# Kernel tuning notes

Measured on AMD Instinct MI355X. Metric: run time of the kernel, lower is better.

## Reference

```python
import jax, jax.numpy as jnp
import numpy as np

B, S, M, H, P, T = 32, 400, 400, 200, 16, 4

def setup_inputs() -> dict:
    key = jax.random.key(0)
    ks = jax.random.split(key, 20)
    sc = 0.05
    inp = {
        'att': jax.random.normal(ks[0], (B, S, M), jnp.float32),
        'mod': jax.random.normal(ks[1], (B, S, M), jnp.float32),
        'mask': jnp.ones((B, S), jnp.float32),
        # LSTMCell: input 2*M, hidden H, gate order i,f,g,o
        'lstm_Wih': jax.random.normal(ks[2], (4 * H, 2 * M), jnp.float32) * sc,
        'lstm_Whh': jax.random.normal(ks[3], (4 * H, H), jnp.float32) * sc,
        'lstm_bih': jnp.zeros((4 * H,), jnp.float32),
        'lstm_bhh': jnp.zeros((4 * H,), jnp.float32),
    }
    for pfx, off in (('s', 4), ('e', 11)):
        inp[pfx + '_rW'] = jax.random.normal(ks[off + 0], (H, 2 * M + H), jnp.float32) * sc
        inp[pfx + '_W1'] = jax.random.normal(ks[off + 1], (P * H, M + H), jnp.float32) * sc
        inp[pfx + '_b1'] = jnp.zeros((P * H,), jnp.float32)
        inp[pfx + '_W2'] = jax.random.normal(ks[off + 2], (P * H, H), jnp.float32) * sc
        inp[pfx + '_b2'] = jnp.zeros((P * H,), jnp.float32)
        inp[pfx + '_W3'] = jax.random.normal(ks[off + 3], (P, 2 * H), jnp.float32) * sc
        inp[pfx + '_b3'] = jnp.zeros((P,), jnp.float32)
    return inp

def _gather(mod, idx):
    # mod:[B,S,M], idx:[B] -> [B,M]
    return jnp.take_along_axis(mod, idx[:, None, None], axis=1)[:, 0, :]

def _lstm_cell(x, h, c, Wih, Whh, bih, bhh):
    g = x @ Wih.T + bih + h @ Whh.T + bhh  # [B,4H]
    i, f, gg, o = jnp.split(g, 4, axis=1)
    c2 = jax.nn.sigmoid(f) * c + jax.nn.sigmoid(i) * jnp.tanh(gg)
    h2 = jax.nn.sigmoid(o) * jnp.tanh(c2)
    return h2, c2

def _hmn(mod, h, us, ue, mask, rW, W1, b1, W2, b2, W3, b3):
    r = jnp.tanh(jnp.concatenate([h, us, ue], 1) @ rW.T)  # [B,H]
    x = jnp.concatenate([mod, jnp.broadcast_to(r[:, None, :], (B, S, H))], 2)  # [B,S,M+H]
    m1 = (x @ W1.T + b1).reshape(B, S, P, H).max(2)   # maxout 1
    m2 = (m1 @ W2.T + b2).reshape(B, S, P, H).max(2)  # maxout 2
    logits = (jnp.concatenate([m1, m2], 2) @ W3.T + b3).max(2)  # [B,S]
    logits = jnp.where(mask > 0, logits, -1e30)
    return jax.nn.log_softmax(logits, axis=1)

def reference(att, mod, mask, lstm_Wih, lstm_Whh, lstm_bih, lstm_bhh,
              s_rW, s_W1, s_b1, s_W2, s_b2, s_W3, s_b3,
              e_rW, e_W1, e_b1, e_W2, e_b2, e_W3, e_b3):
    s_prev = jnp.zeros((B,), jnp.int32)
    e_prev = jnp.sum(mask, 1).astype(jnp.int32) - 1
    h = jnp.zeros((B, H), mod.dtype)
    c = jnp.zeros((B, H), mod.dtype)
    log_p1s, log_p2s = [], []
    for _ in range(T):
        u_s = _gather(mod, s_prev)
        u_e = _gather(mod, e_prev)
        h, c = _lstm_cell(jnp.concatenate([u_s, u_e], 1), h, c,
                          lstm_Wih, lstm_Whh, lstm_bih, lstm_bhh)
        lp1 = _hmn(mod, h, u_s, u_e, mask, s_rW, s_W1, s_b1, s_W2, s_b2, s_W3, s_b3)
        s_prev = jnp.argmax(lp1, axis=1).astype(jnp.int32)
        u_s = _gather(mod, s_prev)
        lp2 = _hmn(mod, h, u_s, u_e, mask, e_rW, e_W1, e_b1, e_W2, e_b2, e_W3, e_b3)
        e_prev = jnp.argmax(lp2, axis=1).astype(jnp.int32)
        log_p1s.append(lp1)
        log_p2s.append(lp2)
    return jnp.stack(log_p1s, 1), jnp.stack(log_p2s, 1)  # each [B,T,S]
```

## Files before the change

### kernel.cpp

```cpp
#include <hip/hip_runtime.h>
#include <math.h>

#define NB 32
#define NS 400
#define NM 400
#define NH 200
#define NP 16
#define NT 4
#define NBS (NB*NS)
#define NPH (NP*NH)
#define NPH2 3328
#define NJT 13
#define NX  (2*NM)
#define NG  (4*NH)
#define NR  (2*NM+NH)
#define K1  1280
#define K2  640

typedef __attribute__((ext_vector_type(8))) short short8v;
typedef __attribute__((ext_vector_type(4))) float f32x4;
typedef __attribute__((ext_vector_type(4))) unsigned short us4;
typedef unsigned short ushort;

__device__ __forceinline__ float sigf(float x){ return 1.0f/(1.0f+expf(-x)); }

__device__ __forceinline__ ushort f2bf(float x){
  union{float f; unsigned u;} v; v.f=x;
  unsigned r = v.u + 0x7fffu + ((v.u>>16)&1u);
  return (ushort)(r>>16);
}
__device__ __forceinline__ float bf2f(ushort u){
  union{float f; unsigned v;} x; x.v = ((unsigned)u)<<16; return x.f;
}
__device__ __forceinline__ float wave_sum(float v){
  #pragma unroll
  for (int o=32;o>0;o>>=1) v += __shfl_xor(v, o);
  return v;
}

__global__ __launch_bounds__(256) void init_kernel(const float* __restrict__ mask,
    float* __restrict__ h, float* __restrict__ c,
    int* __restrict__ sprev, int* __restrict__ eprev){
  int b = blockIdx.x, tid = threadIdx.x;
  __shared__ float red[256];
  float s = 0.f;
  for (int i=tid;i<NS;i+=256) s += mask[(size_t)b*NS+i];
  red[tid]=s; __syncthreads();
  for (int st=128;st>0;st>>=1){ if(tid<st) red[tid]+=red[tid+st]; __syncthreads(); }
  if (tid==0){ sprev[b]=0; eprev[b]=(int)red[0]-1; }
  for (int i=tid;i<NH;i+=256){ h[(size_t)b*NH+i]=0.f; c[(size_t)b*NH+i]=0.f; }
}

__global__ __launch_bounds__(256) void conv_mod_k(const float* __restrict__ in, ushort* __restrict__ out){
  for (size_t i = (size_t)blockIdx.x*256+threadIdx.x; i < (size_t)NBS*K1; i += (size_t)gridDim.x*256){
    int r = (int)(i/K1), k = (int)(i%K1);
    ushort v = 0;
    if (k < 3*NM){
      float x = in[(size_t)r*NM + (k % NM)];
      ushort h = f2bf(x);
      v = (k < NM || k >= 2*NM) ? h : f2bf(x - bf2f(h));
    }
    out[i] = v;
  }
}
__global__ __launch_bounds__(256) void conv_w1_k(const float* __restrict__ in, ushort* __restrict__ out){
  for (size_t i = (size_t)blockIdx.x*256+threadIdx.x; i < (size_t)NPH2*K1; i += (size_t)gridDim.x*256){
    int jp = (int)(i/K1), k = (int)(i%K1);
    ushort v = 0;
    if (jp < NPH && k < 3*NM){
      int j = (jp&15)*NH + (jp>>4);
      float x = in[(size_t)j*(NM+NH) + (k % NM)];
      ushort h = f2bf(x);
      v = (k < 2*NM) ? h : f2bf(x - bf2f(h));
    }
    out[i] = v;
  }
}
__global__ __launch_bounds__(256) void conv_w2_k(const float* __restrict__ in, ushort* __restrict__ out){
  for (size_t i = (size_t)blockIdx.x*256+threadIdx.x; i < (size_t)NPH2*K2; i += (size_t)gridDim.x*256){
    int jp = (int)(i/K2), k = (int)(i%K2);
    ushort v = 0;
    if (jp < NPH && k < 3*NH){
      int j = (jp&15)*NH + (jp>>4);
      float x = in[(size_t)j*NH + (k % NH)];
      ushort h = f2bf(x);
      v = (k < 2*NH) ? h : f2bf(x - bf2f(h));
    }
    out[i] = v;
  }
}
__global__ __launch_bounds__(256) void conv_w1r_k(const float* __restrict__ in, float* __restrict__ out){
  for (size_t i = (size_t)blockIdx.x*256+threadIdx.x; i < (size_t)NH*NPH; i += (size_t)gridDim.x*256){
    int k = (int)(i/NPH), jp = (int)(i%NPH);
    int hh = jp>>4, p = jp&15, j = p*NH + hh;
    out[i] = in[(size_t)j*(NM+NH) + NM + k];
  }
}
__global__ __launch_bounds__(256) void permv_k(const float* __restrict__ in, float* __restrict__ out){
  int i = blockIdx.x*256+threadIdx.x;
  if (i < NPH) out[(i%NH)*NP + i/NH] = in[i];
  else if (i < NPH2) out[i] = 0.f;
}
__global__ __launch_bounds__(256) void pad_zero_k(ushort* __restrict__ p, int stride, int start, int width, int rows){
  for (size_t i = (size_t)blockIdx.x*256+threadIdx.x; i < (size_t)rows*width; i += (size_t)gridDim.x*256){
    int r = (int)(i/width), j = (int)(i%width);
    p[(size_t)r*stride + start + j] = 0;
  }
}

__global__ __launch_bounds__(256) void lstm_gates(const float* __restrict__ mod,
    const int* __restrict__ sprev, const int* __restrict__ eprev,
    const float* __restrict__ h,
    const float* __restrict__ Wih, const float* __restrict__ Whh,
    const float* __restrict__ bih, const float* __restrict__ bhh,
    float* __restrict__ gs){
  int b=blockIdx.x, tid=threadIdx.x;
  __shared__ float xs[NX+NH];
  const float* us = mod + ((size_t)b*NS + sprev[b])*NM;
  const float* ue = mod + ((size_t)b*NS + eprev[b])*NM;
  for (int i=tid;i<NM;i+=256){ xs[i]=us[i]; xs[NM+i]=ue[i]; }
  for (int i=tid;i<NH;i+=256) xs[NX+i]=h[(size_t)b*NH+i];
  __syncthreads();
  int w=tid>>6, lane=tid&63;
  int j = blockIdx.y*4 + w;
  const float* wih = Wih + (size_t)j*NX;
  const float* whh = Whh + (size_t)j*NH;
  float acc=0.f;
  for (int k=lane;k<NX;k+=64) acc += xs[k]*wih[k];
  for (int k=lane;k<NH;k+=64) acc += xs[NX+k]*whh[k];
  acc = wave_sum(acc);
  if (lane==0) gs[(size_t)b*NG+j] = acc + bih[j] + bhh[j];
}
__global__ __launch_bounds__(256) void lstm_update(const float* __restrict__ gs,
    float* __restrict__ h, float* __restrict__ c){
  int b=blockIdx.x, j=threadIdx.x;
  if (j<NH){
    float iv=gs[(size_t)b*NG+j], fv=gs[(size_t)b*NG+NH+j];
    float gv=gs[(size_t)b*NG+2*NH+j], ov=gs[(size_t)b*NG+3*NH+j];
    float c2 = sigf(fv)*c[(size_t)b*NH+j] + sigf(iv)*tanhf(gv);
    c[(size_t)b*NH+j]=c2;
    h[(size_t)b*NH+j]=sigf(ov)*tanhf(c2);
  }
}

__global__ __launch_bounds__(256) void r_kernel(const float* __restrict__ mod,
    const int* __restrict__ sprev, const int* __restrict__ eprev,
    const float* __restrict__ h, const float* __restrict__ rW,
    float* __restrict__ rbuf){
  int b=blockIdx.x, tid=threadIdx.x;
  __shared__ float zs[NR];
  const float* us = mod + ((size_t)b*NS + sprev[b])*NM;
  const float* ue = mod + ((size_t)b*NS + eprev[b])*NM;
  for (int i=tid;i<NH;i+=256) zs[i]=h[(size_t)b*NH+i];
  for (int i=tid;i<NM;i+=256){ zs[NH+i]=us[i]; zs[NH+NM+i]=ue[i]; }
  __syncthreads();
  int w=tid>>6, lane=tid&63;
  int j = blockIdx.y*4 + w;
  const float* wr = rW + (size_t)j*NR;
  float acc=0.f;
  for (int k=lane;k<NR;k+=64) acc += zs[k]*wr[k];
  acc = wave_sum(acc);
  if (lane==0) rbuf[(size_t)b*NH+j] = tanhf(acc);
}

__global__ __launch_bounds__(256) void prer_kernel(const float* __restrict__ rbuf,
    const float* __restrict__ W1rT, const float* __restrict__ b1p,
    float* __restrict__ prer){
  int b=blockIdx.x, tid=threadIdx.x;
  __shared__ float rs[NH];
  if (tid < NH) rs[tid] = rbuf[(size_t)b*NH+tid];
  __syncthreads();
  int jp = blockIdx.y*256 + tid;
  if (jp < NPH2){
    float acc = 0.f;
    if (jp < NPH){
      acc = b1p[jp];
      #pragma unroll 8
      for (int k=0;k<NH;k++) acc += rs[k]*W1rT[(size_t)k*NPH + jp];
    }
    prer[(size_t)b*NPH2 + jp] = acc;
  }
}

template<int MODE>
__global__ __launch_bounds__(512, 2) void gemm_fused(
    const ushort* __restrict__ A, const ushort* __restrict__ W,
    const float* __restrict__ bias, void* __restrict__ outp, int itb){
  constexpr int LDK = (MODE==1) ? K2 : K1;
  constexpr int NTI = LDK/32;
  __shared__ __align__(16) ushort As[4][256*32];
  __shared__ __align__(16) ushort Bs[4][256*32];
  __shared__ float biasLds[2][256];
  __shared__ float outT[256][16];
  const int tid = threadIdx.x;
  const int nwg = gridDim.x;
  const int q = nwg >> 3, r = nwg & 7;
  const int xcd = blockIdx.x & 7, sub = blockIdx.x >> 3;
  const int wkid = (xcd < r) ? (xcd*(q+1) + sub) : (r*(q+1) + (xcd-r)*q + sub);
  const int i0 = (itb + wkid / NJT) * 256, j0 = (wkid % NJT) * 256;
  const int b0 = i0/NS;
  if (MODE==0){
    if (tid<256) biasLds[0][tid] = bias[(size_t)b0*NPH2 + j0 + tid];
    else { int b1r=(i0+255)/NS; biasLds[1][tid-256] = bias[(size_t)b1r*NPH2 + j0 + (tid-256)]; }
  } else if (MODE==1){
    if (tid<256) biasLds[0][tid] = bias[j0+tid];
  }
  const int w = tid>>6, l = tid&63;
  const int wr = w>>2, wc = w&3;
  const int fr = l&15, fk = l>>4;
  const int srow = w*32 + (l>>2);
  const int sslot = l&3;
  const int swzc = (sslot ^ ((srow>>1)&3))*8;
  const ushort* gA0 = A + (size_t)(i0+srow)*LDK + swzc;
  const ushort* gB0 = W + (size_t)(j0+srow)*LDK + swzc;
  const int ldsOff = srow*32 + sslot*8;
  auto stage = [&](int slot, int kt){
    const ushort* a = gA0 + kt*32;
    const ushort* b = gB0 + kt*32;
    __builtin_amdgcn_global_load_lds((const __attribute__((address_space(1))) void*)a,
        (__attribute__((address_space(3))) void*)(&As[slot][ldsOff]), 16, 0, 0);
    __builtin_amdgcn_global_load_lds((const __attribute__((address_space(1))) void*)(a + 16*LDK),
        (__attribute__((address_space(3))) void*)(&As[slot][ldsOff + 16*32]), 16, 0, 0);
    __builtin_amdgcn_global_load_lds((const __attribute__((address_space(1))) void*)b,
        (__attribute__((address_space(3))) void*)(&Bs[slot][ldsOff]), 16, 0, 0);
    __builtin_amdgcn_global_load_lds((const __attribute__((address_space(1))) void*)(b + 16*LDK),
        (__attribute__((address_space(3))) void*)(&Bs[slot][ldsOff + 16*32]), 16, 0, 0);
  };
  f32x4 acc[8][4] = {};
  stage(0,0); stage(1,1); stage(2,2);
  for (int t=0; t<NTI; t++){
    if (t+2 < NTI)      asm volatile("s_waitcnt vmcnt(8)\n\ts_barrier" ::: "memory");
    else if (t+1 < NTI) asm volatile("s_waitcnt vmcnt(4)\n\ts_barrier" ::: "memory");
    else                asm volatile("s_waitcnt vmcnt(0)\n\ts_barrier" ::: "memory");
    const int s = t&3;
    short8v a[8], b[4];
    #pragma unroll
    for (int m=0;m<8;m++){
      int row = wr*128 + m*16 + fr;
      a[m] = *(const short8v*)&As[s][row*32 + ((fk ^ ((row>>1)&3))*8)];
    }
    #pragma unroll
    for (int n=0;n<4;n++){
      int row = wc*64 + n*16 + fr;
      b[n] = *(const short8v*)&Bs[s][row*32 + ((fk ^ ((row>>1)&3))*8)];
    }
    if (t+3 < NTI) stage((t+3)&3, t+3);
    __builtin_amdgcn_s_setprio(1);
    #pragma unroll
    for (int m=0;m<8;m++)
      #pragma unroll
      for (int n=0;n<4;n++)
        acc[m][n] = __builtin_amdgcn_mfma_f32_16x16x32_bf16(a[m], b[n], acc[m][n], 0,0,0);
    __builtin_amdgcn_s_setprio(0);
  }
  if (MODE==2){
    float* o = (float*)outp;
    #pragma unroll
    for (int m=0;m<8;m++){
      #pragma unroll
      for (int n=0;n<4;n++){
        int col = j0 + wc*64 + n*16 + fr;
        if (col < NPH){
          int rbase = i0 + wr*128 + m*16 + fk*4;
          #pragma unroll
          for (int reg=0;reg<4;reg++)
            o[(size_t)(rbase+reg)*NPH + col] = acc[m][n][reg];
        }
      }
    }
    return;
  }
  __syncthreads();
  const int blim = (b0+1)*NS;
  #pragma unroll
  for (int m=0;m<8;m++){
    #pragma unroll
    for (int n=0;n<4;n++){
      int colL = wc*64 + n*16 + fr;
      int rbase = wr*128 + m*16 + fk*4;
      #pragma unroll
      for (int reg=0; reg<4; reg++){
        int rowL = rbase + reg;
        float bv = (MODE==0 && (i0+rowL) >= blim) ? biasLds[1][colL] : biasLds[0][colL];
        float v = acc[m][n][reg] + bv;
        v = fmaxf(v, __shfl_xor(v,1));
        v = fmaxf(v, __shfl_xor(v,2));
        v = fmaxf(v, __shfl_xor(v,4));
        v = fmaxf(v, __shfl_xor(v,8));
        if (fr==0) outT[rowL][wc*4+n] = v;
      }
    }
  }
  __syncthreads();
  {
    int rowL = tid>>1;
    int hloc0 = (tid&1)*8;
    int hg0 = (j0>>4) + hloc0;
    if (hg0 < NH){
      int absrow = i0 + rowL;
      float v[8];
      #pragma unroll
      for (int qq=0;qq<8;qq++) v[qq] = outT[rowL][hloc0+qq];
      if (MODE==0){
        ushort* o = (ushort*)outp + (size_t)absrow*K2 + hg0;
        ushort hi[8], lo[8];
        #pragma unroll
        for (int qq=0;qq<8;qq++){ hi[qq]=f2bf(v[qq]); lo[qq]=f2bf(v[qq]-bf2f(hi[qq])); }
        *(us4*)(o)        = (us4){hi[0],hi[1],hi[2],hi[3]};
        *(us4*)(o+4)      = (us4){hi[4],hi[5],hi[6],hi[7]};
        *(us4*)(o+NH)     = (us4){lo[0],lo[1],lo[2],lo[3]};
        *(us4*)(o+NH+4)   = (us4){lo[4],lo[5],lo[6],lo[7]};
        *(us4*)(o+2*NH)   = (us4){hi[0],hi[1],hi[2],hi[3]};
        *(us4*)(o+2*NH+4) = (us4){hi[4],hi[5],hi[6],hi[7]};
      } else {
        float* o = (float*)outp + (size_t)absrow*NH + hg0;
        *(f32x4*)o     = (f32x4){v[0],v[1],v[2],v[3]};
        *(f32x4*)(o+4) = (f32x4){v[4],v[5],v[6],v[7]};
      }
    }
  }
}

__global__ __launch_bounds__(256) void maxp_kernel(const float* __restrict__ premod,
    const float* __restrict__ prer, ushort* __restrict__ m1e){
  int i = blockIdx.x;
  int b = i / NS;
  int h = threadIdx.x;
  if (h >= NH) return;
  const float* pm = premod + (size_t)i*NPH + h*16;
  const float* pr = prer + (size_t)b*NPH2 + h*16;
  float v = -INFINITY;
  #pragma unroll
  for (int p=0;p<16;p+=4){
    f32x4 a = *(const f32x4*)(pm+p);
    f32x4 c = *(const f32x4*)(pr+p);
    v = fmaxf(v, fmaxf(fmaxf(a.x+c.x, a.y+c.y), fmaxf(a.z+c.z, a.w+c.w)));
  }
  ushort hi = f2bf(v), lo = f2bf(v - bf2f(hi));
  ushort* o = m1e + (size_t)i*K2;
  o[h] = hi; o[NH+h] = lo; o[2*NH+h] = hi;
}

__global__ __launch_bounds__(256) void logits_main(const ushort* __restrict__ m1e,
    const float* __restrict__ m2, const float* __restrict__ W3, const float* __restrict__ b3,
    const float* __restrict__ mask, float* __restrict__ lg){
  int b=blockIdx.x;
  int s=blockIdx.y*256+threadIdx.x;
  if (s >= NS) return;
  const ushort* a = m1e + (size_t)(b*NS+s)*K2;
  const float4* d = (const float4*)(m2 + (size_t)(b*NS+s)*NH);
  float acc[NP];
  #pragma unroll
  for (int p=0;p<NP;p++) acc[p]=b3[p];
  for (int k=0;k<NH/4;k++){
    us4 hv = *(const us4*)(a + 4*k);
    us4 lv = *(const us4*)(a + NH + 4*k);
    float4 dv = d[k];
    float a0=bf2f(hv.x)+bf2f(lv.x), a1=bf2f(hv.y)+bf2f(lv.y);
    float a2=bf2f(hv.z)+bf2f(lv.z), a3=bf2f(hv.w)+bf2f(lv.w);
    #pragma unroll
    for (int p=0;p<NP;p++){
      const float* wp = W3 + p*(2*NH) + 4*k;
      acc[p] += a0*wp[0]+a1*wp[1]+a2*wp[2]+a3*wp[3];
      const float* w2 = wp + NH;
      acc[p] += dv.x*w2[0]+dv.y*w2[1]+dv.z*w2[2]+dv.w*w2[3];
    }
  }
  float best=acc[0];
  #pragma unroll
  for (int p=1;p<NP;p++) best=fmaxf(best,acc[p]);
  lg[(size_t)b*NS+s] = (mask[(size_t)b*NS+s] > 0.f) ? best : -1e30f;
}

__global__ __launch_bounds__(256) void logits_fin(const float* __restrict__ lg,
    float* __restrict__ out, int t, int* __restrict__ prevIdx){
  int b=blockIdx.x, tid=threadIdx.x;
  __shared__ float rv[256]; __shared__ int ri[256]; __shared__ float sv[256];
  float bv=-INFINITY; int bi=NS;
  for (int s=tid;s<NS;s+=256){ float v=lg[(size_t)b*NS+s]; if (v>bv){bv=v;bi=s;} }
  rv[tid]=bv; ri[tid]=bi; __syncthreads();
  for (int st=128;st>0;st>>=1){
    if (tid<st){
      float v2=rv[tid+st]; int i2=ri[tid+st];
      if (v2>rv[tid] || (v2==rv[tid] && i2<ri[tid])){ rv[tid]=v2; ri[tid]=i2; }
    }
    __syncthreads();
  }
  float mx = rv[0];
  float ps=0.f;
  for (int s=tid;s<NS;s+=256) ps += expf(lg[(size_t)b*NS+s]-mx);
  sv[tid]=ps; __syncthreads();
  for (int st=128;st>0;st>>=1){ if (tid<st) sv[tid]+=sv[tid+st]; __syncthreads(); }
  float lse = mx + logf(sv[0]);
  for (int s=tid;s<NS;s+=256) out[((size_t)b*NT + t)*NS + s] = lg[(size_t)b*NS+s]-lse;
  if (tid==0) prevIdx[b]=ri[0];
}

extern "C" void kernel_launch(void* const* d_in, const int* in_sizes, int n_in,
                              void* d_out, int out_size, void* d_ws, size_t ws_size,
                              hipStream_t stream){
  const float* mod  = (const float*)d_in[1];
  const float* mask = (const float*)d_in[2];
  const float* Wih  = (const float*)d_in[3];
  const float* Whh  = (const float*)d_in[4];
  const float* bih  = (const float*)d_in[5];
  const float* bhh  = (const float*)d_in[6];
  const float* rW[2] = {(const float*)d_in[7],  (const float*)d_in[14]};
  const float* W1[2] = {(const float*)d_in[8],  (const float*)d_in[15]};
  const float* b1[2] = {(const float*)d_in[9],  (const float*)d_in[16]};
  const float* W2[2] = {(const float*)d_in[10], (const float*)d_in[17]};
  const float* b2[2] = {(const float*)d_in[11], (const float*)d_in[18]};
  const float* W3[2] = {(const float*)d_in[12], (const float*)d_in[19]};
  const float* b3[2] = {(const float*)d_in[13], (const float*)d_in[20]};
  float* out[2];
  out[0] = (float*)d_out;
  out[1] = out[0] + (size_t)NB*NT*NS;

  float* wsf = (float*)d_ws;
  size_t off = 0;
  auto carve = [&](size_t n)->size_t{ size_t o=off; off += (n + 63) & ~(size_t)63; return o; };
  float* hbuf   = wsf + carve((size_t)NB*NH);
  float* cbuf   = wsf + carve((size_t)NB*NH);
  float* prer   = wsf + carve((size_t)NB*NPH2);
  int*   sprev  = (int*)(wsf + carve(128));
  int*   eprev  = sprev + 32;
  float* m2f    = wsf + carve((size_t)NBS*NH);
  float* b2p[2] = {wsf + carve(NPH2), wsf + carve(NPH2)};
  float* b1p[2] = {wsf + carve(NPH2), wsf + carve(NPH2)};
  float* rbuf   = wsf + carve((size_t)NB*NH);
  float* gsbuf  = wsf + carve((size_t)NB*NG);
  float* lgbuf  = wsf + carve((size_t)NB*NS);
  float* W1rT[2]= {wsf + carve((size_t)NH*NPH), wsf + carve((size_t)NH*NPH)};
  ushort* modExp   = (ushort*)(wsf + carve((size_t)NBS*K1/2));
  ushort* W1exp[2] = {(ushort*)(wsf + carve((size_t)NPH2*K1/2)),
                      (ushort*)(wsf + carve((size_t)NPH2*K1/2))};
  ushort* W2exp[2] = {(ushort*)(wsf + carve((size_t)NPH2*K2/2)),
                      (ushort*)(wsf + carve((size_t)NPH2*K2/2))};
  ushort* m1exp    = (ushort*)(wsf + carve((size_t)NBS*K2/2));

  size_t availF = ws_size / 4;
  const size_t margin = 4096;
  int Xh[2] = {0, 0};
  float* premod[2] = {nullptr, nullptr};
  for (int net=0; net<2; net++){
    long rem = (long)availF - (long)off - (long)margin;
    long rows = rem > 0 ? rem / NPH : 0;
    rows = (rows / 256) * 256;
    if (rows > NBS) rows = NBS;
    if (rows >= 256){
      Xh[net] = (int)rows;
      premod[net] = wsf + carve((size_t)rows * NPH);
    }
  }

  init_kernel<<<NB, 256, 0, stream>>>(mask, hbuf, cbuf, sprev, eprev);
  conv_mod_k<<<2048, 256, 0, stream>>>(mod, modExp);
  pad_zero_k<<<256, 256, 0, stream>>>(m1exp, K2, 3*NH, K2-3*NH, NBS);
  for (int net=0; net<2; net++){
    conv_w1_k<<<2048, 256, 0, stream>>>(W1[net], W1exp[net]);
    conv_w2_k<<<1024, 256, 0, stream>>>(W2[net], W2exp[net]);
    conv_w1r_k<<<1024, 256, 0, stream>>>(W1[net], W1rT[net]);
    permv_k<<<(NPH2+255)/256, 256, 0, stream>>>(b2[net], b2p[net]);
    permv_k<<<(NPH2+255)/256, 256, 0, stream>>>(b1[net], b1p[net]);
  }
  for (int net=0; net<2; net++)
    if (Xh[net] > 0)
      gemm_fused<2><<<(Xh[net]/256)*NJT, 512, 0, stream>>>(modExp, W1exp[net], nullptr,
                                                           (void*)premod[net], 0);

  const int GFULL = (NBS/256) * NJT;
  for (int t=0; t<NT; t++){
    lstm_gates<<<dim3(NB, NG/4), 256, 0, stream>>>(mod, sprev, eprev, hbuf,
                                                   Wih, Whh, bih, bhh, gsbuf);
    lstm_update<<<NB, 256, 0, stream>>>(gsbuf, hbuf, cbuf);
    for (int net=0; net<2; net++){
      r_kernel<<<dim3(NB, NH/4), 256, 0, stream>>>(mod, sprev, eprev, hbuf, rW[net], rbuf);
      prer_kernel<<<dim3(NB, NPH2/256), 256, 0, stream>>>(rbuf, W1rT[net], b1p[net], prer);
      int X = Xh[net];
      if (X > 0)
        maxp_kernel<<<X, 256, 0, stream>>>(premod[net], prer, m1exp);
      if (X < NBS)
        gemm_fused<0><<<((NBS-X)/256)*NJT, 512, 0, stream>>>(modExp, W1exp[net], prer,
                                                             (void*)m1exp, X/256);
      gemm_fused<1><<<GFULL, 512, 0, stream>>>(m1exp, W2exp[net], b2p[net], (void*)m2f, 0);
      logits_main<<<dim3(NB, 2), 256, 0, stream>>>(m1exp, m2f, W3[net], b3[net], mask, lgbuf);
      logits_fin<<<NB, 256, 0, stream>>>(lgbuf, out[net], t, net==0 ? sprev : eprev);
    }
  }
}
```

Measured before the change: 2.771 ms.

## Store bf16 hi/lo split once and reuse A/W fragments across three MFMA products

The split-bf16 operands were stored as three concatenated segments (hi,lo,hi against hi,hi,lo), so the GEMM ran over K=3x. Now each operand keeps only hi and lo segments, and the GEMM loads both into LDS and issues the three cross products (a0*w0, a1*w0, a0*w1) from shared fragments. This cuts global and LDS traffic per unit of work and shrinks the workspace buffers. The pipeline depth drops from 4 to 2 stages and an extra barrier is added per iteration, and the outT buffer now shares its storage with the tiles.

```diff
diff --git a/kernel.cpp b/kernel.cpp
--- a/kernel.cpp
+++ b/kernel.cpp
@@ -14,8 +14,10 @@
 #define NX  (2*NM)
 #define NG  (4*NH)
 #define NR  (2*NM+NH)
-#define K1  1280
-#define K2  640
+#define SG1 416
+#define SK1 832
+#define SG2 224
+#define SK2 448
 
 typedef __attribute__((ext_vector_type(8))) short short8v;
 typedef __attribute__((ext_vector_type(4))) float f32x4;
@@ -52,39 +54,46 @@
 }
 
 __global__ __launch_bounds__(256) void conv_mod_k(const float* __restrict__ in, ushort* __restrict__ out){
-  for (size_t i = (size_t)blockIdx.x*256+threadIdx.x; i < (size_t)NBS*K1; i += (size_t)gridDim.x*256){
-    int r = (int)(i/K1), k = (int)(i%K1);
+  for (size_t i = (size_t)blockIdx.x*256+threadIdx.x; i < (size_t)NBS*SK1; i += (size_t)gridDim.x*256){
+    int r = (int)(i/SK1), k = (int)(i%SK1);
     ushort v = 0;
-    if (k < 3*NM){
-      float x = in[(size_t)r*NM + (k % NM)];
-      ushort h = f2bf(x);
-      v = (k < NM || k >= 2*NM) ? h : f2bf(x - bf2f(h));
+    if (k < 400){
+      float x = in[(size_t)r*NM + k]; v = f2bf(x);
+    } else if (k >= SG1 && k < SG1+400){
+      float x = in[(size_t)r*NM + (k-SG1)];
+      ushort h = f2bf(x); v = f2bf(x - bf2f(h));
     }
     out[i] = v;
   }
 }
 __global__ __launch_bounds__(256) void conv_w1_k(const float* __restrict__ in, ushort* __restrict__ out){
-  for (size_t i = (size_t)blockIdx.x*256+threadIdx.x; i < (size_t)NPH2*K1; i += (size_t)gridDim.x*256){
-    int jp = (int)(i/K1), k = (int)(i%K1);
+  for (size_t i = (size_t)blockIdx.x*256+threadIdx.x; i < (size_t)NPH2*SK1; i += (size_t)gridDim.x*256){
+    int jp = (int)(i/SK1), k = (int)(i%SK1);
     ushort v = 0;
-    if (jp < NPH && k < 3*NM){
+    if (jp < NPH){
       int j = (jp&15)*NH + (jp>>4);
-      float x = in[(size_t)j*(NM+NH) + (k % NM)];
-      ushort h = f2bf(x);
-      v = (k < 2*NM) ? h : f2bf(x - bf2f(h));
+      if (k < 400){
+        v = f2bf(in[(size_t)j*(NM+NH) + k]);
+      } else if (k >= SG1 && k < SG1+400){
+        float x = in[(size_t)j*(NM+NH) + (k-SG1)];
+        ushort h = f2bf(x); v = f2bf(x - bf2f(h));
+      }
     }
     out[i] = v;
   }
 }
 __global__ __launch_bounds__(256) void conv_w2_k(const float* __restrict__ in, ushort* __restrict__ out){
-  for (size_t i = (size_t)blockIdx.x*256+threadIdx.x; i < (size_t)NPH2*K2; i += (size_t)gridDim.x*256){
-    int jp = (int)(i/K2), k = (int)(i%K2);
+  for (size_t i = (size_t)blockIdx.x*256+threadIdx.x; i < (size_t)NPH2*SK2; i += (size_t)gridDim.x*256){
+    int jp = (int)(i/SK2), k = (int)(i%SK2);
     ushort v = 0;
-    if (jp < NPH && k < 3*NH){
+    if (jp < NPH){
       int j = (jp&15)*NH + (jp>>4);
-      float x = in[(size_t)j*NH + (k % NH)];
-      ushort h = f2bf(x);
-      v = (k < 2*NH) ? h : f2bf(x - bf2f(h));
+      if (k < 200){
+        v = f2bf(in[(size_t)j*NH + k]);
+      } else if (k >= SG2 && k < SG2+200){
+        float x = in[(size_t)j*NH + (k-SG2)];
+        ushort h = f2bf(x); v = f2bf(x - bf2f(h));
+      }
     }
     out[i] = v;
   }
@@ -186,12 +195,14 @@
 __global__ __launch_bounds__(512, 2) void gemm_fused(
     const ushort* __restrict__ A, const ushort* __restrict__ W,
     const float* __restrict__ bias, void* __restrict__ outp, int itb){
-  constexpr int LDK = (MODE==1) ? K2 : K1;
-  constexpr int NTI = LDK/32;
-  __shared__ __align__(16) ushort As[4][256*32];
-  __shared__ __align__(16) ushort Bs[4][256*32];
+  constexpr int SEG = (MODE==1) ? SG2 : SG1;
+  constexpr int LDK = 2*SEG;
+  constexpr int NKT = SEG/32;
+  struct SMs { ushort A0[2][256*32]; ushort A1[2][256*32];
+               ushort W0[2][256*32]; ushort W1[2][256*32]; };
+  union SMu { SMs s; float outT[256][16]; };
+  __shared__ SMu sm;
   __shared__ float biasLds[2][256];
-  __shared__ float outT[256][16];
   const int tid = threadIdx.x;
   const int nwg = gridDim.x;
   const int q = nwg >> 3, r = nwg & 7;
@@ -211,47 +222,78 @@
   const int srow = w*32 + (l>>2);
   const int sslot = l&3;
   const int swzc = (sslot ^ ((srow>>1)&3))*8;
-  const ushort* gA0 = A + (size_t)(i0+srow)*LDK + swzc;
-  const ushort* gB0 = W + (size_t)(j0+srow)*LDK + swzc;
+  const ushort* gA = A + (size_t)(i0+srow)*LDK + swzc;
+  const ushort* gB = W + (size_t)(j0+srow)*LDK + swzc;
   const int ldsOff = srow*32 + sslot*8;
   auto stage = [&](int slot, int kt){
-    const ushort* a = gA0 + kt*32;
-    const ushort* b = gB0 + kt*32;
-    __builtin_amdgcn_global_load_lds((const __attribute__((address_space(1))) void*)a,
-        (__attribute__((address_space(3))) void*)(&As[slot][ldsOff]), 16, 0, 0);
-    __builtin_amdgcn_global_load_lds((const __attribute__((address_space(1))) void*)(a + 16*LDK),
-        (__attribute__((address_space(3))) void*)(&As[slot][ldsOff + 16*32]), 16, 0, 0);
-    __builtin_amdgcn_global_load_lds((const __attribute__((address_space(1))) void*)b,
-        (__attribute__((address_space(3))) void*)(&Bs[slot][ldsOff]), 16, 0, 0);
-    __builtin_amdgcn_global_load_lds((const __attribute__((address_space(1))) void*)(b + 16*LDK),
-        (__attribute__((address_space(3))) void*)(&Bs[slot][ldsOff + 16*32]), 16, 0, 0);
+    const ushort* pa0 = gA + kt*32;
+    const ushort* pa1 = gA + SEG + kt*32;
+    const ushort* pw0 = gB + kt*32;
+    const ushort* pw1 = gB + SEG + kt*32;
+    __builtin_amdgcn_global_load_lds((const __attribute__((address_space(1))) void*)pa0,
+        (__attribute__((address_space(3))) void*)(&sm.s.A0[slot][ldsOff]), 16, 0, 0);
+    __builtin_amdgcn_global_load_lds((const __attribute__((address_space(1))) void*)(pa0 + 16*LDK),
+        (__attribute__((address_space(3))) void*)(&sm.s.A0[slot][ldsOff + 512]), 16, 0, 0);
+    __builtin_amdgcn_global_load_lds((const __attribute__((address_space(1))) void*)pa1,
+        (__attribute__((address_space(3))) void*)(&sm.s.A1[slot][ldsOff]), 16, 0, 0);
+    __builtin_amdgcn_global_load_lds((const __attribute__((address_space(1))) void*)(pa1 + 16*LDK),
+        (__attribute__((address_space(3))) void*)(&sm.s.A1[slot][ldsOff + 512]), 16, 0, 0);
+    __builtin_amdgcn_global_load_lds((const __attribute__((address_space(1))) void*)pw0,
+        (__attribute__((address_space(3))) void*)(&sm.s.W0[slot][ldsOff]), 16, 0, 0);
+    __builtin_amdgcn_global_load_lds((const __attribute__((address_space(1))) void*)(pw0 + 16*LDK),
+        (__attribute__((address_space(3))) void*)(&sm.s.W0[slot][ldsOff + 512]), 16, 0, 0);
+    __builtin_amdgcn_global_load_lds((const __attribute__((address_space(1))) void*)pw1,
+        (__attribute__((address_space(3))) void*)(&sm.s.W1[slot][ldsOff]), 16, 0, 0);
+    __builtin_amdgcn_global_load_lds((const __attribute__((address_space(1))) void*)(pw1 + 16*LDK),
+        (__attribute__((address_space(3))) void*)(&sm.s.W1[slot][ldsOff + 512]), 16, 0, 0);
   };
   f32x4 acc[8][4] = {};
-  stage(0,0); stage(1,1); stage(2,2);
-  for (int t=0; t<NTI; t++){
-    if (t+2 < NTI)      asm volatile("s_waitcnt vmcnt(8)\n\ts_barrier" ::: "memory");
-    else if (t+1 < NTI) asm volatile("s_waitcnt vmcnt(4)\n\ts_barrier" ::: "memory");
-    else                asm volatile("s_waitcnt vmcnt(0)\n\ts_barrier" ::: "memory");
-    const int s = t&3;
-    short8v a[8], b[4];
+  stage(0,0);
+  if (NKT > 1) stage(1,1);
+  for (int t=0; t<NKT; t++){
+    const int s = t&1;
+    if (t+1 < NKT) asm volatile("s_waitcnt vmcnt(8)\n\ts_barrier" ::: "memory");
+    else           asm volatile("s_waitcnt vmcnt(0)\n\ts_barrier" ::: "memory");
+    short8v a0[8], a1[8], w0v[4], w1v[4];
     #pragma unroll
     for (int m=0;m<8;m++){
       int row = wr*128 + m*16 + fr;
-      a[m] = *(const short8v*)&As[s][row*32 + ((fk ^ ((row>>1)&3))*8)];
+      a0[m] = *(const short8v*)&sm.s.A0[s][row*32 + ((fk ^ ((row>>1)&3))<<3)];
     }
     #pragma unroll
     for (int n=0;n<4;n++){
       int row = wc*64 + n*16 + fr;
-      b[n] = *(const short8v*)&Bs[s][row*32 + ((fk ^ ((row>>1)&3))*8)];
-    }
-    if (t+3 < NTI) stage((t+3)&3, t+3);
+      int co = (fk ^ ((row>>1)&3))<<3;
+      w0v[n] = *(const short8v*)&sm.s.W0[s][row*32 + co];
+      w1v[n] = *(const short8v*)&sm.s.W1[s][row*32 + co];
+    }
     __builtin_amdgcn_s_setprio(1);
     #pragma unroll
     for (int m=0;m<8;m++)
       #pragma unroll
       for (int n=0;n<4;n++)
-        acc[m][n] = __builtin_amdgcn_mfma_f32_16x16x32_bf16(a[m], b[n], acc[m][n], 0,0,0);
+        acc[m][n] = __builtin_amdgcn_mfma_f32_16x16x32_bf16(a0[m], w0v[n], acc[m][n], 0,0,0);
     __builtin_amdgcn_s_setprio(0);
+    #pragma unroll
+    for (int m=0;m<8;m++){
+      int row = wr*128 + m*16 + fr;
+      a1[m] = *(const short8v*)&sm.s.A1[s][row*32 + ((fk ^ ((row>>1)&3))<<3)];
+    }
+    __builtin_amdgcn_s_setprio(1);
+    #pragma unroll
+    for (int m=0;m<8;m++)
+      #pragma unroll
+      for (int n=0;n<4;n++)
+        acc[m][n] = __builtin_amdgcn_mfma_f32_16x16x32_bf16(a1[m], w0v[n], acc[m][n], 0,0,0);
+    #pragma unroll
+    for (int m=0;m<8;m++)
+      #pragma unroll
+      for (int n=0;n<4;n++)
+        acc[m][n] = __builtin_amdgcn_mfma_f32_16x16x32_bf16(a0[m], w1v[n], acc[m][n], 0,0,0);
+    __builtin_amdgcn_s_setprio(0);
+    asm volatile("s_waitcnt lgkmcnt(0)" ::: "memory");
+    __builtin_amdgcn_s_barrier();
+    if (t+2 < NKT) stage(s, t+2);
   }
   if (MODE==2){
     float* o = (float*)outp;
@@ -287,7 +329,7 @@
         v = fmaxf(v, __shfl_xor(v,2));
         v = fmaxf(v, __shfl_xor(v,4));
         v = fmaxf(v, __shfl_xor(v,8));
-        if (fr==0) outT[rowL][wc*4+n] = v;
+        if (fr==0) sm.outT[rowL][wc*4+n] = v;
       }
     }
   }
@@ -300,18 +342,16 @@
       int absrow = i0 + rowL;
       float v[8];
       #pragma unroll
-      for (int qq=0;qq<8;qq++) v[qq] = outT[rowL][hloc0+qq];
+      for (int qq=0;qq<8;qq++) v[qq] = sm.outT[rowL][hloc0+qq];
       if (MODE==0){
-        ushort* o = (ushort*)outp + (size_t)absrow*K2 + hg0;
+        ushort* o = (ushort*)outp + (size_t)absrow*SK2 + hg0;
         ushort hi[8], lo[8];
         #pragma unroll
         for (int qq=0;qq<8;qq++){ hi[qq]=f2bf(v[qq]); lo[qq]=f2bf(v[qq]-bf2f(hi[qq])); }
         *(us4*)(o)        = (us4){hi[0],hi[1],hi[2],hi[3]};
         *(us4*)(o+4)      = (us4){hi[4],hi[5],hi[6],hi[7]};
-        *(us4*)(o+NH)     = (us4){lo[0],lo[1],lo[2],lo[3]};
-        *(us4*)(o+NH+4)   = (us4){lo[4],lo[5],lo[6],lo[7]};
-        *(us4*)(o+2*NH)   = (us4){hi[0],hi[1],hi[2],hi[3]};
-        *(us4*)(o+2*NH+4) = (us4){hi[4],hi[5],hi[6],hi[7]};
+        *(us4*)(o+SG2)    = (us4){lo[0],lo[1],lo[2],lo[3]};
+        *(us4*)(o+SG2+4)  = (us4){lo[4],lo[5],lo[6],lo[7]};
       } else {
         float* o = (float*)outp + (size_t)absrow*NH + hg0;
         *(f32x4*)o     = (f32x4){v[0],v[1],v[2],v[3]};
@@ -337,8 +377,8 @@
     v = fmaxf(v, fmaxf(fmaxf(a.x+c.x, a.y+c.y), fmaxf(a.z+c.z, a.w+c.w)));
   }
   ushort hi = f2bf(v), lo = f2bf(v - bf2f(hi));
-  ushort* o = m1e + (size_t)i*K2;
-  o[h] = hi; o[NH+h] = lo; o[2*NH+h] = hi;
+  ushort* o = m1e + (size_t)i*SK2;
+  o[h] = hi; o[SG2+h] = lo;
 }
 
 __global__ __launch_bounds__(256) void logits_main(const ushort* __restrict__ m1e,
@@ -347,14 +387,14 @@
   int b=blockIdx.x;
   int s=blockIdx.y*256+threadIdx.x;
   if (s >= NS) return;
-  const ushort* a = m1e + (size_t)(b*NS+s)*K2;
+  const ushort* a = m1e + (size_t)(b*NS+s)*SK2;
   const float4* d = (const float4*)(m2 + (size_t)(b*NS+s)*NH);
   float acc[NP];
   #pragma unroll
   for (int p=0;p<NP;p++) acc[p]=b3[p];
   for (int k=0;k<NH/4;k++){
     us4 hv = *(const us4*)(a + 4*k);
-    us4 lv = *(const us4*)(a + NH + 4*k);
+    us4 lv = *(const us4*)(a + SG2 + 4*k);
     float4 dv = d[k];
     float a0=bf2f(hv.x)+bf2f(lv.x), a1=bf2f(hv.y)+bf2f(lv.y);
     float a2=bf2f(hv.z)+bf2f(lv.z), a3=bf2f(hv.w)+bf2f(lv.w);
@@ -431,12 +471,12 @@
   float* gsbuf  = wsf + carve((size_t)NB*NG);
   float* lgbuf  = wsf + carve((size_t)NB*NS);
   float* W1rT[2]= {wsf + carve((size_t)NH*NPH), wsf + carve((size_t)NH*NPH)};
-  ushort* modExp   = (ushort*)(wsf + carve((size_t)NBS*K1/2));
-  ushort* W1exp[2] = {(ushort*)(wsf + carve((size_t)NPH2*K1/2)),
-                      (ushort*)(wsf + carve((size_t)NPH2*K1/2))};
-  ushort* W2exp[2] = {(ushort*)(wsf + carve((size_t)NPH2*K2/2)),
-                      (ushort*)(wsf + carve((size_t)NPH2*K2/2))};
-  ushort* m1exp    = (ushort*)(wsf + carve((size_t)NBS*K2/2));
+  ushort* modExp   = (ushort*)(wsf + carve((size_t)NBS*SK1/2));
+  ushort* W1exp[2] = {(ushort*)(wsf + carve((size_t)NPH2*SK1/2)),
+                      (ushort*)(wsf + carve((size_t)NPH2*SK1/2))};
+  ushort* W2exp[2] = {(ushort*)(wsf + carve((size_t)NPH2*SK2/2)),
+                      (ushort*)(wsf + carve((size_t)NPH2*SK2/2))};
+  ushort* m1exp    = (ushort*)(wsf + carve((size_t)NBS*SK2/2));
 
   size_t availF = ws_size / 4;
   const size_t margin = 4096;
@@ -455,10 +495,11 @@
 
   init_kernel<<<NB, 256, 0, stream>>>(mask, hbuf, cbuf, sprev, eprev);
   conv_mod_k<<<2048, 256, 0, stream>>>(mod, modExp);
-  pad_zero_k<<<256, 256, 0, stream>>>(m1exp, K2, 3*NH, K2-3*NH, NBS);
+  pad_zero_k<<<128, 256, 0, stream>>>(m1exp, SK2, 200, SG2-200, NBS);
+  pad_zero_k<<<128, 256, 0, stream>>>(m1exp, SK2, SG2+200, SG2-200, NBS);
   for (int net=0; net<2; net++){
-    conv_w1_k<<<2048, 256, 0, stream>>>(W1[net], W1exp[net]);
-    conv_w2_k<<<1024, 256, 0, stream>>>(W2[net], W2exp[net]);
+    conv_w1_k<<<1024, 256, 0, stream>>>(W1[net], W1exp[net]);
+    conv_w2_k<<<512, 256, 0, stream>>>(W2[net], W2exp[net]);
     conv_w1r_k<<<1024, 256, 0, stream>>>(W1[net], W1rT[net]);
     permv_k<<<(NPH2+255)/256, 256, 0, stream>>>(b2[net], b2p[net]);
     permv_k<<<(NPH2+255)/256, 256, 0, stream>>>(b1[net], b1p[net]);
```

After: 3.300 ms. +19.1%, slower.
